# Kernel optimization log

Measured on AMD Instinct MI355X. Metric: run time of the kernel, lower is better.

The kernel has to match this reference:

```python
import jax, jax.numpy as jnp
import numpy as np

B, S, H, I = 2, 2048, 4096, 16384
EPS = 1e-12


def setup_inputs() -> dict:
    key = jax.random.key(0)
    ks = jax.random.split(key, 8)
    w_scale = 0.02
    return {
        "input": jax.random.normal(ks[0], (B, S, H), jnp.float32),
        "residual": jax.random.normal(ks[1], (B, S, H), jnp.float32),
        "bias": jax.random.normal(ks[2], (H,), jnp.float32) * w_scale,
        "attn_nw": jnp.ones((H,), jnp.float32),
        "attn_nb": jnp.zeros((H,), jnp.float32),
        "inter_w": jax.random.normal(ks[3], (I, H), jnp.float32) * w_scale,
        "inter_b": jax.random.normal(ks[4], (I,), jnp.float32) * w_scale,
        "output_w": jax.random.normal(ks[5], (H, I), jnp.float32) * w_scale,
        "output_b": jax.random.normal(ks[6], (H,), jnp.float32) * w_scale,
    }


def reference(input, residual, bias, attn_nw, attn_nb, inter_w, inter_b, output_w, output_b):
    # Fused mlp_gemm: residual_add = input + residual + attn-output bias
    residual_add = input + residual + bias  # [B,S,H]
    # LayerNorm over hidden dim with attn_nw/attn_nb
    mean = jnp.mean(residual_add, axis=-1, keepdims=True)
    var = jnp.var(residual_add, axis=-1, keepdims=True)
    ln = (residual_add - mean) * jax.lax.rsqrt(var + EPS) * attn_nw + attn_nb
    # Intermediate GEMM + bias + GELU (DeepSpeed uses tanh-approx gelu)
    inter = jax.nn.gelu(jnp.einsum("bsh,ih->bsi", ln, inter_w) + inter_b, approximate=True)
    # Output projection (vector_matmul)
    out = jnp.einsum("bsi,hi->bsh", inter, output_w)
    # bias_residual: add residual_add and output bias
    return out + residual_add + output_b
```

## Files before the change

### kernel.cpp

```cpp
#include <hip/hip_runtime.h>
#include <hip/hip_bf16.h>
#include <cstdint>
#include <math.h>

typedef __attribute__((ext_vector_type(4))) float f32x4;
typedef __attribute__((ext_vector_type(8))) __bf16 bf16x8;

__device__ __forceinline__ unsigned short f2bf(float f) {
    union { float f; unsigned u; } v; v.f = f;
    unsigned u = v.u + 0x7fffu + ((v.u >> 16) & 1u);
    return (unsigned short)(u >> 16);
}

__device__ __forceinline__ float gelu_tanh(float x) {
    float x3 = x * x * x;
    float t = tanhf(0.7978845608028654f * (x + 0.044715f * x3));
    return 0.5f * x * (1.0f + t);
}

__device__ __forceinline__ void gload_lds16(const void* g, void* l) {
    __builtin_amdgcn_global_load_lds(
        (__attribute__((address_space(1))) void*)(uintptr_t)g,
        (__attribute__((address_space(3))) void*)(unsigned)(uintptr_t)l,
        16, 0, 0);
}

__global__ __launch_bounds__(256)
void fused_add_ln(const float* __restrict__ in, const float* __restrict__ res,
                  const float* __restrict__ bias, const float* __restrict__ nw,
                  const float* __restrict__ nb, float* __restrict__ resadd,
                  unsigned short* __restrict__ lnout, int H) {
    const int row = blockIdx.x;
    const int tid = threadIdx.x;
    const size_t base = (size_t)row * H;
    float v[16];
    float s = 0.f, ss = 0.f;
#pragma unroll
    for (int i = 0; i < 4; ++i) {
        int idx = (i * 256 + tid) * 4;
        float4 a = *(const float4*)(in + base + idx);
        float4 b = *(const float4*)(res + base + idx);
        float4 c = *(const float4*)(bias + idx);
        float x0 = a.x + b.x + c.x, x1 = a.y + b.y + c.y;
        float x2 = a.z + b.z + c.z, x3 = a.w + b.w + c.w;
        v[i * 4 + 0] = x0; v[i * 4 + 1] = x1; v[i * 4 + 2] = x2; v[i * 4 + 3] = x3;
        s += x0 + x1 + x2 + x3;
        ss += x0 * x0 + x1 * x1 + x2 * x2 + x3 * x3;
    }
#pragma unroll
    for (int off = 32; off > 0; off >>= 1) {
        s += __shfl_down(s, off);
        ss += __shfl_down(ss, off);
    }
    __shared__ float red[8];
    const int w = tid >> 6;
    if ((tid & 63) == 0) { red[w] = s; red[4 + w] = ss; }
    __syncthreads();
    s = red[0] + red[1] + red[2] + red[3];
    ss = red[4] + red[5] + red[6] + red[7];
    const float mean = s / H;
    const float var = ss / H - mean * mean;
    const float rstd = rsqrtf(var + 1e-12f);
#pragma unroll
    for (int i = 0; i < 4; ++i) {
        int idx = (i * 256 + tid) * 4;
        float4 wv = *(const float4*)(nw + idx);
        float4 bv = *(const float4*)(nb + idx);
        float4 r;
        r.x = v[i * 4 + 0]; r.y = v[i * 4 + 1]; r.z = v[i * 4 + 2]; r.w = v[i * 4 + 3];
        *(float4*)(resadd + base + idx) = r;
        ushort4 o;
        o.x = f2bf((r.x - mean) * rstd * wv.x + bv.x);
        o.y = f2bf((r.y - mean) * rstd * wv.y + bv.y);
        o.z = f2bf((r.z - mean) * rstd * wv.z + bv.z);
        o.w = f2bf((r.w - mean) * rstd * wv.w + bv.w);
        *(ushort4*)(lnout + base + idx) = o;
    }
}

__global__ __launch_bounds__(256)
void cast_w(const float* __restrict__ w, unsigned short* __restrict__ o, long long n4) {
    long long i = (long long)blockIdx.x * 256 + threadIdx.x;
    if (i >= n4) return;
    float4 f = *(const float4*)(w + i * 4);
    ushort4 u;
    u.x = f2bf(f.x); u.y = f2bf(f.y); u.z = f2bf(f.z); u.w = f2bf(f.w);
    *(ushort4*)(o + i * 4) = u;
}

#define GBM 256
#define GBN 256

#define STAGE(s, mat, h, T) do {                                              \
    const unsigned short* _src = ((mat) ? pB : pA)                            \
        + (size_t)((h) * 128) * K + (size_t)(T) * 64;                         \
    char* _dst = ldsc + (s) * 65536 + (mat) * 32768 + (h) * 16384 + dOff;     \
    gload_lds16(_src, _dst);                                                  \
    gload_lds16(_src + (size_t)64 * K, _dst + 8192);                          \
} while (0)

#define STG(s, T) do { STAGE(s, 0, 0, T); STAGE(s, 0, 1, T);                  \
                       STAGE(s, 1, 0, T); STAGE(s, 1, 1, T); } while (0)

#define RD_B(s) do {                                                          \
    _Pragma("unroll")                                                         \
    for (int ni = 0; ni < 4; ++ni)                                            \
        _Pragma("unroll")                                                     \
        for (int kk = 0; kk < 2; ++kk)                                        \
            bq[ni][kk] = *(const bf16x8*)(ldsc + (s) * 65536 + 32768          \
                + ((wc * 64 + ni * 16 + lrow) << 7) + ckk[kk]);               \
} while (0)

#define RD_A(bk, q, s) do {                                                   \
    _Pragma("unroll")                                                         \
    for (int m2 = 0; m2 < 2; ++m2)                                            \
        _Pragma("unroll")                                                     \
        for (int kk = 0; kk < 2; ++kk)                                        \
            aq[bk][m2][kk] = *(const bf16x8*)(ldsc + (s) * 65536              \
                + ((wr * 128 + ((q) * 2 + m2) * 16 + lrow) << 7) + ckk[kk]);  \
} while (0)

#define MF(q, bk) do {                                                        \
    __builtin_amdgcn_s_setprio(1);                                            \
    _Pragma("unroll")                                                         \
    for (int m2 = 0; m2 < 2; ++m2)                                            \
        _Pragma("unroll")                                                     \
        for (int ni = 0; ni < 4; ++ni)                                        \
            _Pragma("unroll")                                                 \
            for (int kk = 0; kk < 2; ++kk)                                    \
                acc[(q) * 2 + m2][ni] = __builtin_amdgcn_mfma_f32_16x16x32_bf16( \
                    aq[bk][m2][kk], bq[ni][kk], acc[(q) * 2 + m2][ni], 0, 0, 0); \
    __builtin_amdgcn_s_setprio(0);                                            \
} while (0)

#define WAITP do { asm volatile("s_waitcnt lgkmcnt(0)" ::: "memory");         \
                   __builtin_amdgcn_sched_barrier(0); } while (0)
#define BAR   asm volatile("s_barrier" ::: "memory")
#define GATE0 asm volatile("s_waitcnt vmcnt(0)" ::: "memory")

template <int EPI>
__global__ __launch_bounds__(512, 2)
void gemm256(const unsigned short* __restrict__ A,
             const unsigned short* __restrict__ B,
             const float* __restrict__ bias_n,
             const float* __restrict__ resadd,
             void* __restrict__ Cout,
             int M, int N, int K) {
    __shared__ unsigned short lds[2][2][2][128 * 64];
    char* ldsc = (char*)&lds[0][0][0][0];
    const int tid = threadIdx.x;
    const int lane = tid & 63;
    const int w = tid >> 6;
    const int wr = w >> 2;
    const int wc = w & 3;

    const int nwg = gridDim.x;
    const int lg = (blockIdx.x & 7) * (nwg >> 3) + (blockIdx.x >> 3);
    const int nbx = N / GBN;
    const int brow = lg / nbx;
    const int bcol = lg % nbx;

    const int srow = tid >> 3;
    const int scol = ((((tid & 7) << 4) ^ ((srow & 7) << 4)) >> 1);
    const unsigned short* pA = A + (size_t)(brow * GBM + srow) * K + scol;
    const unsigned short* pB = B + (size_t)(bcol * GBN + srow) * K + scol;
    const int dOff = tid * 16;

    const int lrow = lane & 15;
    int ckk[2];
    ckk[0] = (((lane >> 4) << 4)) ^ ((lrow & 7) << 4);
    ckk[1] = ckk[0] ^ 64;

    f32x4 acc[8][4] = {};
    bf16x8 aq[2][2][2];
    bf16x8 bq[4][2];

    const int NT = K / 64;
    const int niter = NT / 2;

    STG(0, 0);
    GATE0; BAR;
    RD_B(0); RD_A(0, 0, 0);

    for (int i = 0; i < niter - 1; ++i) {
        const int T1 = 2 * i + 1, T2 = 2 * i + 2;
        WAITP; MF(0, 0); RD_A(1, 1, 0); STG(1, T1);
        WAITP; MF(1, 1); RD_A(0, 2, 0);
        WAITP; MF(2, 0); RD_A(1, 3, 0);
        WAITP; MF(3, 1); GATE0; BAR; RD_B(1); RD_A(0, 0, 1);
        WAITP; MF(0, 0); RD_A(1, 1, 1); STG(0, T2);
        WAITP; MF(1, 1); RD_A(0, 2, 1);
        WAITP; MF(2, 0); RD_A(1, 3, 1);
        WAITP; MF(3, 1); GATE0; BAR; RD_B(0); RD_A(0, 0, 0);
    }
    {
        WAITP; MF(0, 0); RD_A(1, 1, 0); STG(1, NT - 1);
        WAITP; MF(1, 1); RD_A(0, 2, 0);
        WAITP; MF(2, 0); RD_A(1, 3, 0);
        WAITP; MF(3, 1); GATE0; BAR; RD_B(1); RD_A(0, 0, 1);
        WAITP; MF(0, 0); RD_A(1, 1, 1);
        WAITP; MF(1, 1); RD_A(0, 2, 1);
        WAITP; MF(2, 0); RD_A(1, 3, 1);
        WAITP; MF(3, 1);
    }

    const int c0 = bcol * GBN + wc * 64 + lrow;
    const int r0 = brow * GBM + wr * 128 + (lane >> 4) * 4;
#pragma unroll
    for (int mi = 0; mi < 8; ++mi) {
#pragma unroll
        for (int j = 0; j < 4; ++j) {
            const int row = r0 + mi * 16 + j;
#pragma unroll
            for (int ni = 0; ni < 4; ++ni) {
                const int col = c0 + ni * 16;
                float x = acc[mi][ni][j] + bias_n[col];
                if (EPI == 0) {
                    ((unsigned short*)Cout)[(size_t)row * N + col] = f2bf(gelu_tanh(x));
                } else {
                    const size_t off = (size_t)row * N + col;
                    ((float*)Cout)[off] = x + resadd[off];
                }
            }
        }
    }
}

extern "C" void kernel_launch(void* const* d_in, const int* in_sizes, int n_in,
                              void* d_out, int out_size, void* d_ws, size_t ws_size,
                              hipStream_t stream) {
    const float* input    = (const float*)d_in[0];
    const float* residual = (const float*)d_in[1];
    const float* bias     = (const float*)d_in[2];
    const float* attn_nw  = (const float*)d_in[3];
    const float* attn_nb  = (const float*)d_in[4];
    const float* inter_w  = (const float*)d_in[5];
    const float* inter_b  = (const float*)d_in[6];
    const float* output_w = (const float*)d_in[7];
    const float* output_b = (const float*)d_in[8];

    const int H = in_sizes[3];
    const int I = in_sizes[6];
    const int T = in_sizes[0] / H;

    char* ws = (char*)d_ws;
    float* resadd      = (float*)ws;
    unsigned short* ln = (unsigned short*)(ws + (size_t)T * H * 4);
    unsigned short* w1 = (unsigned short*)((char*)ln + (size_t)T * H * 2);
    unsigned short* w2 = w1 + (size_t)I * H;
    unsigned short* act = w2 + (size_t)H * I;

    fused_add_ln<<<T, 256, 0, stream>>>(input, residual, bias, attn_nw, attn_nb,
                                        resadd, ln, H);

    {
        long long n4 = (long long)I * H / 4;
        int blocks = (int)((n4 + 255) / 256);
        cast_w<<<blocks, 256, 0, stream>>>(inter_w, w1, n4);
        cast_w<<<blocks, 256, 0, stream>>>(output_w, w2, n4);
    }

    {
        dim3 grid((T / GBM) * (I / GBN));
        gemm256<0><<<grid, 512, 0, stream>>>(ln, w1, inter_b, nullptr, act, T, I, H);
    }

    {
        dim3 grid((T / GBM) * (H / GBN));
        gemm256<1><<<grid, 512, 0, stream>>>(act, w2, output_b, resadd, d_out, T, H, I);
    }
}
```

Measured before the change: 1.199 ms.

## Restructure GEMM main loop into fine-grained per-half staging with barrier per phase

Result: faster. 1.098 ms (-8.4%).

```diff
diff --git a/kernel.cpp b/kernel.cpp
--- a/kernel.cpp
+++ b/kernel.cpp
@@ -99,9 +99,6 @@
     gload_lds16(_src + (size_t)64 * K, _dst + 8192);                          \
 } while (0)
 
-#define STG(s, T) do { STAGE(s, 0, 0, T); STAGE(s, 0, 1, T);                  \
-                       STAGE(s, 1, 0, T); STAGE(s, 1, 1, T); } while (0)
-
 #define RD_B(s) do {                                                          \
     _Pragma("unroll")                                                         \
     for (int ni = 0; ni < 4; ++ni)                                            \
@@ -111,31 +108,32 @@
                 + ((wc * 64 + ni * 16 + lrow) << 7) + ckk[kk]);               \
 } while (0)
 
-#define RD_A(bk, q, s) do {                                                   \
+#define RD_A(q, s) do {                                                       \
     _Pragma("unroll")                                                         \
     for (int m2 = 0; m2 < 2; ++m2)                                            \
         _Pragma("unroll")                                                     \
         for (int kk = 0; kk < 2; ++kk)                                        \
-            aq[bk][m2][kk] = *(const bf16x8*)(ldsc + (s) * 65536              \
+            aq[m2][kk] = *(const bf16x8*)(ldsc + (s) * 65536                  \
                 + ((wr * 128 + ((q) * 2 + m2) * 16 + lrow) << 7) + ckk[kk]);  \
 } while (0)
 
-#define MF(q, bk) do {                                                        \
+#define MF(q) do {                                                            \
     __builtin_amdgcn_s_setprio(1);                                            \
     _Pragma("unroll")                                                         \
-    for (int m2 = 0; m2 < 2; ++m2)                                            \
+    for (int kk = 0; kk < 2; ++kk)                                            \
         _Pragma("unroll")                                                     \
-        for (int ni = 0; ni < 4; ++ni)                                        \
+        for (int m2 = 0; m2 < 2; ++m2)                                        \
             _Pragma("unroll")                                                 \
-            for (int kk = 0; kk < 2; ++kk)                                    \
+            for (int ni = 0; ni < 4; ++ni)                                    \
                 acc[(q) * 2 + m2][ni] = __builtin_amdgcn_mfma_f32_16x16x32_bf16( \
-                    aq[bk][m2][kk], bq[ni][kk], acc[(q) * 2 + m2][ni], 0, 0, 0); \
+                    aq[m2][kk], bq[ni][kk], acc[(q) * 2 + m2][ni], 0, 0, 0);  \
     __builtin_amdgcn_s_setprio(0);                                            \
 } while (0)
 
-#define WAITP do { asm volatile("s_waitcnt lgkmcnt(0)" ::: "memory");         \
-                   __builtin_amdgcn_sched_barrier(0); } while (0)
+#define LG do { asm volatile("s_waitcnt lgkmcnt(0)" ::: "memory");            \
+                __builtin_amdgcn_sched_barrier(0); } while (0)
 #define BAR   asm volatile("s_barrier" ::: "memory")
+#define GATE2 asm volatile("s_waitcnt vmcnt(2)" ::: "memory")
 #define GATE0 asm volatile("s_waitcnt vmcnt(0)" ::: "memory")
 
 template <int EPI>
@@ -172,36 +170,38 @@
     ckk[1] = ckk[0] ^ 64;
 
     f32x4 acc[8][4] = {};
-    bf16x8 aq[2][2][2];
+    bf16x8 aq[2][2];
     bf16x8 bq[4][2];
 
     const int NT = K / 64;
     const int niter = NT / 2;
 
-    STG(0, 0);
+    STAGE(0, 1, 0, 0); STAGE(0, 1, 1, 0);
+    STAGE(0, 0, 0, 0); STAGE(0, 0, 1, 0);
+    STAGE(1, 1, 0, 1); STAGE(1, 1, 1, 1);
     GATE0; BAR;
-    RD_B(0); RD_A(0, 0, 0);
 
     for (int i = 0; i < niter - 1; ++i) {
-        const int T1 = 2 * i + 1, T2 = 2 * i + 2;
-        WAITP; MF(0, 0); RD_A(1, 1, 0); STG(1, T1);
-        WAITP; MF(1, 1); RD_A(0, 2, 0);
-        WAITP; MF(2, 0); RD_A(1, 3, 0);
-        WAITP; MF(3, 1); GATE0; BAR; RD_B(1); RD_A(0, 0, 1);
-        WAITP; MF(0, 0); RD_A(1, 1, 1); STG(0, T2);
-        WAITP; MF(1, 1); RD_A(0, 2, 1);
-        WAITP; MF(2, 0); RD_A(1, 3, 1);
-        WAITP; MF(3, 1); GATE0; BAR; RD_B(0); RD_A(0, 0, 0);
-    }
-    {
-        WAITP; MF(0, 0); RD_A(1, 1, 0); STG(1, NT - 1);
-        WAITP; MF(1, 1); RD_A(0, 2, 0);
-        WAITP; MF(2, 0); RD_A(1, 3, 0);
-        WAITP; MF(3, 1); GATE0; BAR; RD_B(1); RD_A(0, 0, 1);
-        WAITP; MF(0, 0); RD_A(1, 1, 1);
-        WAITP; MF(1, 1); RD_A(0, 2, 1);
-        WAITP; MF(2, 0); RD_A(1, 3, 1);
-        WAITP; MF(3, 1);
+        const int T1 = 2 * i + 1, T2 = 2 * i + 2, T3 = 2 * i + 3;
+        RD_B(0); RD_A(0, 0);        BAR; STAGE(1, 0, 0, T1); LG; MF(0);
+        RD_A(1, 0);                 BAR; STAGE(1, 0, 1, T1); LG; MF(1);
+        RD_A(2, 0);                 BAR; STAGE(0, 1, 0, T2); LG; MF(2);
+        RD_A(3, 0); GATE2;          BAR; STAGE(0, 1, 1, T2); LG; MF(3);
+        RD_B(1); RD_A(0, 1);        BAR; STAGE(0, 0, 0, T2); LG; MF(0);
+        RD_A(1, 1);                 BAR; STAGE(0, 0, 1, T2); LG; MF(1);
+        RD_A(2, 1);                 BAR; STAGE(1, 1, 0, T3); LG; MF(2);
+        RD_A(3, 1); GATE2;          BAR; STAGE(1, 1, 1, T3); LG; MF(3);
+    }
+    {
+        const int T1 = NT - 1;
+        RD_B(0); RD_A(0, 0);        BAR; STAGE(1, 0, 0, T1); LG; MF(0);
+        RD_A(1, 0);                 BAR; STAGE(1, 0, 1, T1); LG; MF(1);
+        RD_A(2, 0);                 BAR;                     LG; MF(2);
+        RD_A(3, 0); GATE0;          BAR;                     LG; MF(3);
+        RD_B(1); RD_A(0, 1);        BAR;                     LG; MF(0);
+        RD_A(1, 1);                 BAR;                     LG; MF(1);
+        RD_A(2, 1);                 BAR;                     LG; MF(2);
+        RD_A(3, 1);                 BAR;                     LG; MF(3);
     }
 
     const int c0 = bcol * GBN + wc * 64 + lrow;
```
